# Kernel tuning notes

Measured on AMD Instinct MI355X. Metric: run time of the kernel, lower is better.

## Reference

```python
import jax, jax.numpy as jnp
import numpy as np

N_PAIR = 32
N_ENTI = 36          # VidVRD object classes (+pad)
N_CLS_TOT = 133      # 132 predicate classes + background id 0
NUM_BASE = 92        # split='base' -> pids 1..92
N_CTX = 8
MAX_L = 40           # GeneralAlproCfg.max_txt_len
D = 768


def setup_inputs() -> dict:
    key = jax.random.key(0)
    ks = jax.random.split(key, 11)
    std = 0.02
    return {
        "so_cls_ids": jax.random.randint(ks[0], (N_PAIR, 2), 0, N_ENTI, dtype=jnp.int64),
        "enti_txt_embds": jax.random.normal(ks[1], (N_ENTI, 256), jnp.float32),
        "prefix_embds": jax.random.normal(ks[2], (N_CLS_TOT, 1, D), jnp.float32) * std,
        "suffix_embds": jax.random.normal(ks[3], (N_CLS_TOT, MAX_L - 1 - N_CTX, D), jnp.float32) * std,
        "token_mask": jnp.ones((N_CLS_TOT, MAX_L), jnp.int32),
        "meta_ctx_embds": jax.random.normal(ks[4], (N_CTX, D), jnp.float32) * std,
        "subj_ctx_embds": jax.random.normal(ks[5], (N_CTX, D), jnp.float32) * std,
        "obj_ctx_embds": jax.random.normal(ks[6], (N_CTX, D), jnp.float32) * std,
        "W1": jax.random.normal(ks[7], (512, 256), jnp.float32) * std,
        "b1": jnp.zeros((256,), jnp.float32),
        "W2": jax.random.normal(ks[8], (256, 2 * D), jnp.float32) * std,
    }


def reference(so_cls_ids, enti_txt_embds, prefix_embds, suffix_embds, token_mask,
              meta_ctx_embds, subj_ctx_embds, obj_ctx_embds, W1, b1, W2):
    n_pair = so_cls_ids.shape[0]
    pids = jnp.arange(1, NUM_BASE + 1)                      # split='base'
    n_cls = NUM_BASE

    # entity text-embedding gather + tiny MLP
    s_embd = enti_txt_embds[so_cls_ids[:, 0]]               # [n_pair, 256]
    o_embd = enti_txt_embds[so_cls_ids[:, 1]]
    so = jnp.concatenate([s_embd, o_embd], axis=-1)         # [n_pair, 512]
    h = jax.nn.relu(so @ W1 + b1)                           # [n_pair, 256]
    so_e = h @ W2                                           # [n_pair, 1536]
    s_q, o_q = so_e[:, :D], so_e[:, D:]

    # softmax attention over meta context (keys = values = meta_ctx_embds)
    scale = 1.0 / jnp.sqrt(jnp.asarray(D, jnp.float32))
    s_att = jax.nn.softmax(s_q @ meta_ctx_embds.T * scale, axis=-1) @ meta_ctx_embds  # [n_pair, D]
    o_att = jax.nn.softmax(o_q @ meta_ctx_embds.T * scale, axis=-1) @ meta_ctx_embds

    s_ctx = subj_ctx_embds[None, :, :] + s_att[:, None, :]  # [n_pair, n_ctx, D]
    o_ctx = obj_ctx_embds[None, :, :] + o_att[:, None, :]

    prefix = prefix_embds[pids]                             # [n_cls, 1, D]
    suffix = suffix_embds[pids]                             # [n_cls, L_suf, D]
    l_suf = suffix.shape[1]

    def build(ctx):
        return jnp.concatenate([
            jnp.broadcast_to(prefix[None], (n_pair, n_cls, 1, D)),
            jnp.broadcast_to(ctx[:, None], (n_pair, n_cls, N_CTX, D)),
            jnp.broadcast_to(suffix[None], (n_pair, n_cls, l_suf, D)),
        ], axis=2).reshape(n_pair * n_cls, MAX_L, D)

    subj_token_embds = build(s_ctx)                         # [n_pair*n_cls, MAX_L, D]
    obj_token_embds = build(o_ctx)
    mask = jnp.tile(token_mask[pids], (n_pair, 1))          # [n_pair*n_cls, MAX_L]
    return subj_token_embds, obj_token_embds, mask
```

## Files before the change

### kernel.cpp

```cpp
#include <hip/hip_runtime.h>
#include <hip/hip_bf16.h>

typedef unsigned int u32;
typedef __attribute__((ext_vector_type(4))) float f32x4;

#define NPAIR 32
#define NCLS  92
#define NCTX  8
#define MAXL  40
#define DIM   768
#define LSUF  31

#define MAT_ELEMS 90439680u
#define MASK_BASE 180879360u
#define NBLK_MAT  5888u
#define MASK_F4   29440u
#define NBLK_MASK 115u

#define WS_ATT  0u
#define WS_H    49152u
#define WS_SOE  57344u

__global__ __launch_bounds__(512) void k_h(
    const int* __restrict__ so_ids,
    const float* __restrict__ enti,
    const float* __restrict__ W1,
    const float* __restrict__ b1,
    float* __restrict__ ws)
{
    const int p = blockIdx.x;
    const int t = threadIdx.x;
    __shared__ float so_vec[512];
    __shared__ float w1part[2][256];
    __shared__ int ids[2];

    if (t == 0) {
        bool is64 = true;
        for (int i = 1; i < 64; i += 2) is64 = is64 && (so_ids[i] == 0);
        if (is64) { ids[0] = so_ids[4 * p];     ids[1] = so_ids[4 * p + 2]; }
        else      { ids[0] = so_ids[2 * p];     ids[1] = so_ids[2 * p + 1]; }
    }
    __syncthreads();
    so_vec[t] = (t < 256) ? enti[ids[0] * 256 + t] : enti[ids[1] * 256 + (t - 256)];
    __syncthreads();

    const int j = t & 255, half = t >> 8;
    const float* w = W1 + (half * 256) * 256 + j;
    const float* sv = so_vec + half * 256;
    float acc = 0.f;
    #pragma unroll 8
    for (int kk = 0; kk < 256; ++kk)
        acc = fmaf(sv[kk], w[(size_t)kk * 256], acc);
    w1part[half][j] = acc;
    __syncthreads();
    if (t < 256)
        ws[WS_H + p * 256 + t] = fmaxf(w1part[0][t] + w1part[1][t] + b1[t], 0.f);
}

__global__ __launch_bounds__(256) void k_soe(
    const float* __restrict__ W2,
    float* __restrict__ ws)
{
    const int p = blockIdx.x / 6;
    const int cc = blockIdx.x % 6;
    const int t = threadIdx.x;
    __shared__ float hl[256];
    hl[t] = ws[WS_H + p * 256 + t];
    __syncthreads();

    const int c = cc * 256 + t;
    const float* w = W2 + c;
    float acc = 0.f;
    #pragma unroll 8
    for (int k = 0; k < 256; ++k)
        acc = fmaf(hl[k], w[(size_t)k * 1536], acc);
    ws[WS_SOE + p * 1536 + c] = acc;
}

__global__ __launch_bounds__(256) void k_att(
    const float* __restrict__ meta,
    float* __restrict__ ws)
{
    const int which = blockIdx.x >> 5;
    const int p = blockIdx.x & 31;
    const int t = threadIdx.x;
    __shared__ float red[8][256];
    __shared__ float probs[8];

    const float* q = ws + WS_SOE + p * 1536 + which * DIM;
    float qr[3];
    #pragma unroll
    for (int i = 0; i < 3; ++i) qr[i] = q[t + 256 * i];

    #pragma unroll
    for (int c = 0; c < 8; ++c) {
        float pp = 0.f;
        #pragma unroll
        for (int i = 0; i < 3; ++i)
            pp = fmaf(qr[i], meta[c * DIM + t + 256 * i], pp);
        red[c][t] = pp;
    }
    __syncthreads();
    for (int s = 128; s > 0; s >>= 1) {
        if (t < s) {
            #pragma unroll
            for (int c = 0; c < 8; ++c)
                red[c][t] += red[c][t + s];
        }
        __syncthreads();
    }
    if (t == 0) {
        const float scale = 0.036084391824351615f;
        float sc[8], m = -1e30f;
        #pragma unroll
        for (int c = 0; c < 8; ++c) { sc[c] = red[c][0] * scale; m = fmaxf(m, sc[c]); }
        float sum = 0.f;
        #pragma unroll
        for (int c = 0; c < 8; ++c) { sc[c] = expf(sc[c] - m); sum += sc[c]; }
        const float inv = 1.f / sum;
        #pragma unroll
        for (int c = 0; c < 8; ++c) probs[c] = sc[c] * inv;
    }
    __syncthreads();
    #pragma unroll
    for (int i = 0; i < 3; ++i) {
        const int d = t + 256 * i;
        float a = 0.f;
        #pragma unroll
        for (int c = 0; c < 8; ++c)
            a = fmaf(probs[c], meta[c * DIM + d], a);
        ws[WS_ATT + (which * NPAIR + p) * DIM + d] = a;
    }
}

__global__ __launch_bounds__(256) void k_build(
    const float* __restrict__ prefix,
    const float* __restrict__ suffix,
    const int* __restrict__ tok_mask,
    const float* __restrict__ sctx,
    const float* __restrict__ octx,
    const float* __restrict__ att,
    float* __restrict__ out)
{
    const u32 bid = blockIdx.x;
    const u32 t = threadIdx.x;

    if (bid < NBLK_MAT) {
        const u32 which = bid / (NPAIR * NCLS);
        const u32 rem = bid - which * (NPAIR * NCLS);
        const u32 pair = rem / NCLS;
        const u32 cls = rem - pair * NCLS;

        __shared__ __align__(16) float attl[DIM];
        for (u32 i = t; i < DIM; i += 256u)
            attl[i] = att[(which * NPAIR + pair) * DIM + i];
        __syncthreads();

        const float* ctx = which ? octx : sctx;
        const f32x4* pre4 = (const f32x4*)(prefix + (cls + 1u) * DIM);
        const f32x4* suf4 = (const f32x4*)(suffix + (size_t)(cls + 1u) * LSUF * DIM);
        f32x4* base4 = (f32x4*)(out + (size_t)which * MAT_ELEMS
                                    + ((size_t)pair * NCLS + cls) * (MAXL * DIM));

        #pragma unroll 6
        for (u32 it = 0; it < 30u; ++it) {
            const u32 chunk = it * 256u + t;
            const u32 tok = chunk / 192u;
            const u32 dpos = chunk - tok * 192u;
            f32x4 v;
            if (tok == 0u) {
                v = pre4[dpos];
            } else if (tok < 9u) {
                v = *(const f32x4*)(ctx + (tok - 1u) * DIM + dpos * 4u)
                  + *(const f32x4*)(attl + dpos * 4u);
            } else {
                v = suf4[(tok - 9u) * 192u + dpos];
            }
            __builtin_nontemporal_store(v, base4 + chunk);
        }
    } else {
        const u32 idx4 = (bid - NBLK_MAT) * 256u + t;
        if (idx4 < MASK_F4) {
            const u32 m = idx4 * 4u;
            f32x4 v;
            #pragma unroll
            for (int j = 0; j < 4; ++j) {
                const u32 i = m + (u32)j;
                const u32 rw = i / 40u;
                const u32 tk = i - rw * 40u;
                const u32 cls = rw % 92u;
                v[j] = (float)tok_mask[(cls + 1u) * 40u + tk];
            }
            __builtin_nontemporal_store(v, (f32x4*)(out + MASK_BASE + m));
        }
    }
}

extern "C" void kernel_launch(void* const* d_in, const int* in_sizes, int n_in,
                              void* d_out, int out_size, void* d_ws, size_t ws_size,
                              hipStream_t stream) {
    const int* so_ids     = (const int*)d_in[0];
    const float* enti     = (const float*)d_in[1];
    const float* prefix   = (const float*)d_in[2];
    const float* suffix   = (const float*)d_in[3];
    const int* tok_mask   = (const int*)d_in[4];
    const float* meta     = (const float*)d_in[5];
    const float* sctx     = (const float*)d_in[6];
    const float* octx     = (const float*)d_in[7];
    const float* W1       = (const float*)d_in[8];
    const float* b1       = (const float*)d_in[9];
    const float* W2       = (const float*)d_in[10];
    float* ws = (float*)d_ws;

    k_h  <<<dim3(NPAIR), dim3(512), 0, stream>>>(so_ids, enti, W1, b1, ws);
    k_soe<<<dim3(192),   dim3(256), 0, stream>>>(W2, ws);
    k_att<<<dim3(64),    dim3(256), 0, stream>>>(meta, ws);
    k_build<<<dim3(NBLK_MAT + NBLK_MASK), dim3(256), 0, stream>>>(
        prefix, suffix, tok_mask, sctx, octx, ws + WS_ATT, (float*)d_out);
}
```

Measured before the change: 173.0 us.

## Split build into ctx and prefix/suffix kernels with shared-memory source reuse

```diff
diff --git a/kernel.cpp b/kernel.cpp
--- a/kernel.cpp
+++ b/kernel.cpp
@@ -13,7 +13,7 @@
 
 #define MAT_ELEMS 90439680u
 #define MASK_BASE 180879360u
-#define NBLK_MAT  5888u
+#define NBLK_D1   1472u
 #define MASK_F4   29440u
 #define NBLK_MASK 115u
 
@@ -133,53 +133,48 @@
     }
 }
 
-__global__ __launch_bounds__(256) void k_build(
+__global__ __launch_bounds__(256) void k_copy(
     const float* __restrict__ prefix,
     const float* __restrict__ suffix,
     const int* __restrict__ tok_mask,
-    const float* __restrict__ sctx,
-    const float* __restrict__ octx,
-    const float* __restrict__ att,
     float* __restrict__ out)
 {
     const u32 bid = blockIdx.x;
     const u32 t = threadIdx.x;
 
-    if (bid < NBLK_MAT) {
-        const u32 which = bid / (NPAIR * NCLS);
-        const u32 rem = bid - which * (NPAIR * NCLS);
-        const u32 pair = rem / NCLS;
-        const u32 cls = rem - pair * NCLS;
-
-        __shared__ __align__(16) float attl[DIM];
-        for (u32 i = t; i < DIM; i += 256u)
-            attl[i] = att[(which * NPAIR + pair) * DIM + i];
+    if (bid < NBLK_D1) {
+        const u32 which = bid / (NCLS * 8u);
+        const u32 rem = bid - which * (NCLS * 8u);
+        const u32 cls = rem / 8u;
+        const u32 tq = rem - cls * 8u;
+
+        __shared__ __align__(16) float srcl[4 * DIM];
+        for (u32 u = t; u < 4u * 192u; u += 256u) {
+            const u32 j = u / 192u;
+            const u32 dpos = u - j * 192u;
+            const u32 rtok = (tq == 0u) ? (j == 0u ? 0u : 8u + j) : (8u + 4u * tq + j);
+            const float* src = (rtok == 0u)
+                ? (prefix + (size_t)(cls + 1u) * DIM + dpos * 4u)
+                : (suffix + ((size_t)(cls + 1u) * LSUF + (rtok - 9u)) * DIM + dpos * 4u);
+            *(f32x4*)(srcl + u * 4u) = *(const f32x4*)src;
+        }
         __syncthreads();
 
-        const float* ctx = which ? octx : sctx;
-        const f32x4* pre4 = (const f32x4*)(prefix + (cls + 1u) * DIM);
-        const f32x4* suf4 = (const f32x4*)(suffix + (size_t)(cls + 1u) * LSUF * DIM);
-        f32x4* base4 = (f32x4*)(out + (size_t)which * MAT_ELEMS
-                                    + ((size_t)pair * NCLS + cls) * (MAXL * DIM));
-
-        #pragma unroll 6
-        for (u32 it = 0; it < 30u; ++it) {
-            const u32 chunk = it * 256u + t;
-            const u32 tok = chunk / 192u;
-            const u32 dpos = chunk - tok * 192u;
-            f32x4 v;
-            if (tok == 0u) {
-                v = pre4[dpos];
-            } else if (tok < 9u) {
-                v = *(const f32x4*)(ctx + (tok - 1u) * DIM + dpos * 4u)
-                  + *(const f32x4*)(attl + dpos * 4u);
-            } else {
-                v = suf4[(tok - 9u) * 192u + dpos];
+        for (u32 pair = 0; pair < NPAIR; ++pair) {
+            float* slab = out + (size_t)which * MAT_ELEMS
+                              + ((size_t)(pair * NCLS + cls) * MAXL) * DIM;
+            #pragma unroll
+            for (u32 uu = 0; uu < 3u; ++uu) {
+                const u32 u = uu * 256u + t;
+                const u32 j = u / 192u;
+                const u32 dpos = u - j * 192u;
+                const u32 rtok = (tq == 0u) ? (j == 0u ? 0u : 8u + j) : (8u + 4u * tq + j);
+                __builtin_nontemporal_store(*(const f32x4*)(srcl + u * 4u),
+                    (f32x4*)(slab + (size_t)rtok * DIM + dpos * 4u));
             }
-            __builtin_nontemporal_store(v, base4 + chunk);
         }
     } else {
-        const u32 idx4 = (bid - NBLK_MAT) * 256u + t;
+        const u32 idx4 = (bid - NBLK_D1) * 256u + t;
         if (idx4 < MASK_F4) {
             const u32 m = idx4 * 4u;
             f32x4 v;
@@ -192,6 +187,44 @@
                 v[j] = (float)tok_mask[(cls + 1u) * 40u + tk];
             }
             __builtin_nontemporal_store(v, (f32x4*)(out + MASK_BASE + m));
+        }
+    }
+}
+
+__global__ __launch_bounds__(256) void k_ctx(
+    const float* __restrict__ sctx,
+    const float* __restrict__ octx,
+    const float* __restrict__ att,
+    float* __restrict__ out)
+{
+    const u32 bid = blockIdx.x;
+    const u32 t = threadIdx.x;
+    const u32 which = bid / 128u;
+    const u32 rem = bid - which * 128u;
+    const u32 pair = rem / 4u;
+    const u32 cg = rem & 3u;
+
+    const float* ctx = which ? octx : sctx;
+    const float* ar = att + (size_t)(which * NPAIR + pair) * DIM;
+
+    __shared__ __align__(16) float sums[8 * DIM];
+    for (u32 u = t; u < 8u * 192u; u += 256u) {
+        const u32 dpos = u % 192u;
+        const f32x4 v = *(const f32x4*)(ctx + (size_t)u * 4u)
+                      + *(const f32x4*)(ar + (size_t)dpos * 4u);
+        *(f32x4*)(sums + u * 4u) = v;
+    }
+    __syncthreads();
+
+    for (u32 c = 0; c < 23u; ++c) {
+        const u32 cls = cg * 23u + c;
+        float* base = out + (size_t)which * MAT_ELEMS
+                          + ((size_t)(pair * NCLS + cls) * MAXL + 1u) * DIM;
+        #pragma unroll
+        for (u32 uu = 0; uu < 6u; ++uu) {
+            const u32 u = uu * 256u + t;
+            __builtin_nontemporal_store(*(const f32x4*)(sums + u * 4u),
+                (f32x4*)(base + (size_t)u * 4u));
         }
     }
 }
@@ -215,6 +248,7 @@
     k_h  <<<dim3(NPAIR), dim3(512), 0, stream>>>(so_ids, enti, W1, b1, ws);
     k_soe<<<dim3(192),   dim3(256), 0, stream>>>(W2, ws);
     k_att<<<dim3(64),    dim3(256), 0, stream>>>(meta, ws);
-    k_build<<<dim3(NBLK_MAT + NBLK_MASK), dim3(256), 0, stream>>>(
-        prefix, suffix, tok_mask, sctx, octx, ws + WS_ATT, (float*)d_out);
-}
+    k_ctx<<<dim3(256),   dim3(256), 0, stream>>>(sctx, octx, ws + WS_ATT, (float*)d_out);
+    k_copy<<<dim3(NBLK_D1 + NBLK_MASK), dim3(256), 0, stream>>>(
+        prefix, suffix, tok_mask, (float*)d_out);
+}
```

After: 171.0 us. No clear change (-1.1%).
